# Optimization experiments

Measured on AMD Instinct MI355X. Metric: run time of the kernel, lower is better.

## Reference

```python
import jax, jax.numpy as jnp
import numpy as np

G, KS = 8, 3          # groups, kernel size
K = KS * KS           # sampling points per group
OM = 32               # per-group offset_mask dim: ceil(3K/8)*8
EPS = 1e-5


def setup_inputs() -> dict:
    key = jax.random.key(0)
    ks = jax.random.split(key, 12)
    N, C, H, W = 4, 128, 64, 64
    x = jax.random.normal(ks[0], (N, C, H, W), jnp.float32)
    w_value = jax.random.normal(ks[1], (C, C), jnp.float32) / np.sqrt(C)
    b_value = jax.random.normal(ks[2], (C,), jnp.float32) * 0.01
    # small offset weights -> modest sampling offsets (real module inits these to 0)
    w_off = jax.random.normal(ks[3], (C, G * OM), jnp.float32) * 0.02
    b_off = jax.random.normal(ks[4], (G * OM,), jnp.float32) * 0.01
    w_out = jax.random.normal(ks[5], (C, C), jnp.float32) / np.sqrt(C)
    b_out = jax.random.normal(ks[6], (C,), jnp.float32) * 0.01
    bn_gamma = jax.random.uniform(ks[7], (C,), jnp.float32, 0.5, 1.5)
    bn_beta = jax.random.normal(ks[8], (C,), jnp.float32) * 0.1
    bn_mean = jax.random.normal(ks[9], (C,), jnp.float32) * 0.1
    bn_var = jax.random.uniform(ks[10], (C,), jnp.float32, 0.5, 1.5)
    return dict(x=x, w_value=w_value, b_value=b_value, w_off=w_off, b_off=b_off,
                w_out=w_out, b_out=b_out, bn_gamma=bn_gamma, bn_beta=bn_beta,
                bn_mean=bn_mean, bn_var=bn_var)


def _dcnv4(x, w_value, b_value, w_off, b_off, w_out, b_out,
           bn_gamma, bn_beta, bn_mean, bn_var):
    N, C, H, W = x.shape
    Cg = C // G
    P = H * W
    xf = x.transpose(0, 2, 3, 1).reshape(N, P, C)              # N,P,C (channels-last tokens)
    val = xf @ w_value + b_value                               # value projection
    om = (xf @ w_off + b_off).reshape(N, P, G, OM)             # offsets+mask (padded to 32)
    offset = om[..., :2 * K].reshape(N, P, G, K, 2)            # (dx, dy) pairs
    mask = om[..., 2 * K:3 * K]                                # modulation, NO softmax (DCNv4)

    # base sampling grid: output pixel + centered 3x3 footprint (stride 1, dil 1)
    py, px = jnp.meshgrid(jnp.arange(H), jnp.arange(W), indexing='ij')
    kk = jnp.arange(KS) - (KS - 1) // 2
    ky, kx = jnp.meshgrid(kk, kk, indexing='ij')
    base_y = (py.reshape(-1)[:, None] + ky.reshape(-1)[None, :]).astype(x.dtype)  # P,K
    base_x = (px.reshape(-1)[:, None] + kx.reshape(-1)[None, :]).astype(x.dtype)
    sy = base_y[None, :, None, :] + offset[..., 1]             # N,P,G,K sampling y
    sx = base_x[None, :, None, :] + offset[..., 0]             # N,P,G,K sampling x

    vflat = val.reshape(N, P, G, Cg).transpose(0, 2, 1, 3)     # N,G,P,Cg

    def gather(iy, ix):
        lin = jnp.clip(iy, 0, H - 1) * W + jnp.clip(ix, 0, W - 1)   # N,P,G,K
        lin = lin.transpose(0, 2, 1, 3).reshape(N, G, P * K)
        g = jnp.take_along_axis(vflat, lin[..., None], axis=2)      # N,G,P*K,Cg
        return g.reshape(N, G, P, K, Cg).transpose(0, 2, 1, 3, 4)   # N,P,G,K,Cg

    y0 = jnp.floor(sy); x0 = jnp.floor(sx)
    ty = sy - y0; tx = sx - x0
    y0i = y0.astype(jnp.int32); x0i = x0.astype(jnp.int32)

    def valid(iy, ix):
        return ((iy >= 0) & (iy < H) & (ix >= 0) & (ix < W)).astype(x.dtype)

    acc = jnp.zeros((N, P, G, K, Cg), x.dtype)
    for dy, dx, wgt in ((0, 0, (1 - ty) * (1 - tx)), (0, 1, (1 - ty) * tx),
                        (1, 0, ty * (1 - tx)), (1, 1, ty * tx)):
        iy, ix = y0i + dy, x0i + dx
        acc = acc + gather(iy, ix) * (wgt * valid(iy, ix))[..., None]

    out = (acc * mask[..., None]).sum(axis=3)                  # aggregate over K -> N,P,G,Cg
    out = out.reshape(N, P, C) @ w_out + b_out                 # output projection
    out = out.reshape(N, H, W, C).transpose(0, 3, 1, 2)        # back to NCHW

    # BatchNorm (inference) + SiLU
    inv = bn_gamma / jnp.sqrt(bn_var + EPS)
    out = out * inv[None, :, None, None] + (bn_beta - bn_mean * inv)[None, :, None, None]
    return out * jax.nn.sigmoid(out)


def reference(x, w_value, b_value, w_off, b_off, w_out, b_out,
              bn_gamma, bn_beta, bn_mean, bn_var):
    return _dcnv4(x, w_value, b_value, w_off, b_off, w_out, b_out,
                  bn_gamma, bn_beta, bn_mean, bn_var)
```

## Files before the change

kernel.cpp:

```cpp
#include <hip/hip_runtime.h>
#include <cstdint>

typedef __bf16 v8bf __attribute__((ext_vector_type(8)));
typedef float f32x4 __attribute__((ext_vector_type(4)));

#define BN_EPS 1e-5f

__device__ __forceinline__ float b2f(uint32_t u) {
    union { uint32_t i; float f; } v; v.i = u << 16; return v.f;
}
__device__ __forceinline__ uint16_t f2b(float f) {
    uint32_t u = __builtin_bit_cast(uint32_t, f);
    u += 0x7fffu + ((u >> 16) & 1u);
    return (uint16_t)(u >> 16);
}

__global__ void prep_transpose_kernel(const float* __restrict__ x,
                                      const float* __restrict__ wv, const float* __restrict__ wo,
                                      const float* __restrict__ wout,
                                      uint16_t* __restrict__ xf, uint16_t* __restrict__ wT) {
    int bid = blockIdx.x;
    if (bid < 512) {
        __shared__ float lds[64 * 65];
        int cb = bid & 1, pb = (bid >> 1) & 63, n = bid >> 7;
        int c0 = cb * 64, p0 = pb * 64;
        int l = threadIdx.x & 63, q = threadIdx.x >> 6;
        const float* xp = x + ((size_t)(n * 128 + c0)) * 4096 + p0;
#pragma unroll
        for (int i = 0; i < 16; i++) {
            int c = i * 4 + q;
            lds[l * 65 + c] = xp[(size_t)c * 4096 + l];
        }
        __syncthreads();
#pragma unroll
        for (int i = 0; i < 16; i++) {
            int pr = i * 4 + q;
            xf[((size_t)(n * 4096 + p0 + pr)) * 128 + c0 + l] = f2b(lds[pr * 65 + l]);
        }
    } else {
        int idx = (bid - 512) * 256 + threadIdx.x;
        if (idx < 512 * 128) {
            int r = idx >> 7, ci = idx & 127;
            float v;
            if (r < 128)      v = wv[ci * 128 + r];
            else if (r < 384) v = wo[ci * 256 + (r - 128)];
            else              v = wout[ci * 128 + (r - 384)];
            wT[idx] = f2b(v);
        }
    }
}

__launch_bounds__(256)
__global__ void gemm1_kernel(const uint16_t* __restrict__ xf, const uint16_t* __restrict__ wT,
                             const float* __restrict__ b_value, const float* __restrict__ b_off,
                             uint16_t* __restrict__ valb, uint16_t* __restrict__ omb) {
    __shared__ __align__(16) uint16_t ldsX[128 * 136];
    __shared__ __align__(16) uint16_t ldsW[64 * 136];
    int ct = blockIdx.x;
    int pt = blockIdx.y;
    int p0 = pt * 128, cbase = ct * 64;
    int tid = threadIdx.x;
    int col16 = tid & 15, rowq = tid >> 4;

    const uint4* xg = (const uint4*)xf;
    uint4* lx = (uint4*)ldsX;
#pragma unroll
    for (int i = 0; i < 8; i++) {
        int row = i * 16 + rowq;
        lx[row * 17 + col16] = xg[(size_t)(p0 + row) * 16 + col16];
    }
    const uint4* wg = (const uint4*)wT;
    uint4* lw = (uint4*)ldsW;
#pragma unroll
    for (int i = 0; i < 4; i++) {
        int row = i * 16 + rowq;
        lw[row * 17 + col16] = wg[(size_t)(cbase + row) * 16 + col16];
    }
    __syncthreads();

    int wv = tid >> 6, lane = tid & 63;
    int ln = lane & 15, quad = lane >> 4;
    int cW = cbase + wv * 16 + quad * 4;
    f32x4 binit;
    if (cW < 128) binit = f32x4{b_value[cW], b_value[cW + 1], b_value[cW + 2], b_value[cW + 3]};
    else          binit = f32x4{b_off[cW - 128], b_off[cW - 127], b_off[cW - 126], b_off[cW - 125]};
    f32x4 acc[8];
#pragma unroll
    for (int t = 0; t < 8; t++) acc[t] = binit;

#pragma unroll
    for (int kk = 0; kk < 4; kk++) {
        v8bf a = *(const v8bf*)&ldsW[(wv * 16 + ln) * 136 + kk * 32 + quad * 8];
#pragma unroll
        for (int t = 0; t < 8; t++) {
            v8bf b = *(const v8bf*)&ldsX[(t * 16 + ln) * 136 + kk * 32 + quad * 8];
            acc[t] = __builtin_amdgcn_mfma_f32_16x16x32_bf16(a, b, acc[t], 0, 0, 0);
        }
    }

    int nimg = p0 >> 12, pin0 = p0 & 4095;
    if (cW < 128) {
        int g = cW >> 4, cg = cW & 15;
#pragma unroll
        for (int t = 0; t < 8; t++) {
            int p = pin0 + t * 16 + ln;
            uint32_t u0 = (uint32_t)f2b(acc[t][0]) | ((uint32_t)f2b(acc[t][1]) << 16);
            uint32_t u1 = (uint32_t)f2b(acc[t][2]) | ((uint32_t)f2b(acc[t][3]) << 16);
            *(uint2*)&valb[(((size_t)(nimg * 8 + g) * 4096 + p) << 4) + cg] = make_uint2(u0, u1);
        }
    } else {
        int j0 = cW - 128;
#pragma unroll
        for (int t = 0; t < 8; t++) {
            int p = pin0 + t * 16 + ln;
            uint32_t u0 = (uint32_t)f2b(acc[t][0]) | ((uint32_t)f2b(acc[t][1]) << 16);
            uint32_t u1 = (uint32_t)f2b(acc[t][2]) | ((uint32_t)f2b(acc[t][3]) << 16);
            *(uint2*)&omb[((size_t)(nimg * 4096 + p) << 8) + j0] = make_uint2(u0, u1);
        }
    }
}

__launch_bounds__(256)
__global__ void gather_gemm3_kernel(const uint16_t* __restrict__ omb, const uint16_t* __restrict__ valb,
                                    const uint16_t* __restrict__ wT,
                                    const float* __restrict__ b_out,
                                    const float* __restrict__ gamma, const float* __restrict__ beta,
                                    const float* __restrict__ mean, const float* __restrict__ var,
                                    float* __restrict__ out) {
    __shared__ __align__(16) uint16_t ldsA[16 * 136];
    __shared__ __align__(16) uint16_t ldsW[128 * 136];
    int pt = blockIdx.x;
    int p0 = pt * 16;
    int n = p0 >> 12, pin0 = p0 & 4095;
    int tid = threadIdx.x;

    {
        int col16 = tid & 15, rowq = tid >> 4;
        const uint4* wg = (const uint4*)wT;
        uint4* lw = (uint4*)ldsW;
#pragma unroll
        for (int i = 0; i < 8; i++) {
            int row = i * 16 + rowq;
            lw[row * 17 + col16] = wg[(size_t)(384 + row) * 16 + col16];
        }
    }

    int pl = tid & 15, g = (tid >> 4) & 7, h = tid >> 7;
    int p = p0 + pl;
    int pin = p & 4095;
    int py = pin >> 6, px = pin & 63;

    const uint16_t* op = omb + ((size_t)p << 8) + g * 32;
    uint4 q0 = *(const uint4*)(op);
    uint4 q1 = *(const uint4*)(op + 8);
    uint4 q2 = *(const uint4*)(op + 16);
    uint2 q3 = *(const uint2*)(op + 24);
    uint32_t w[14] = {q0.x, q0.y, q0.z, q0.w, q1.x, q1.y, q1.z, q1.w,
                      q2.x, q2.y, q2.z, q2.w, q3.x, q3.y};
    float o[28];
#pragma unroll
    for (int i = 0; i < 14; i++) { o[2 * i] = b2f(w[i] & 0xffff); o[2 * i + 1] = b2f(w[i] >> 16); }

    float acc[8];
#pragma unroll
    for (int i = 0; i < 8; i++) acc[i] = 0.f;

    const uint4* vb = (const uint4*)(valb + ((size_t)(n * 8 + g) << 16)) + h;
#pragma unroll
    for (int k = 0; k < 9; k++) {
        float sx = (float)(px + (k % 3) - 1) + o[2 * k];
        float sy = (float)(py + (k / 3) - 1) + o[2 * k + 1];
        float m = o[18 + k];
        float x0f = floorf(sx), y0f = floorf(sy);
        float tx = sx - x0f, ty = sy - y0f;
        int x0 = (int)x0f, y0 = (int)y0f;
        float wy[2] = {m * (1.f - ty), m * ty};
        float wx[2] = {1.f - tx, tx};
#pragma unroll
        for (int dy = 0; dy < 2; dy++) {
            int iy = y0 + dy;
            if (iy < 0 || iy > 63) continue;
#pragma unroll
            for (int dx = 0; dx < 2; dx++) {
                int ix = x0 + dx;
                if (ix < 0 || ix > 63) continue;
                float wgt = wy[dy] * wx[dx];
                uint4 v0 = vb[((size_t)(iy * 64 + ix)) * 2];
                acc[0] += wgt * b2f(v0.x & 0xffff); acc[1] += wgt * b2f(v0.x >> 16);
                acc[2] += wgt * b2f(v0.y & 0xffff); acc[3] += wgt * b2f(v0.y >> 16);
                acc[4] += wgt * b2f(v0.z & 0xffff); acc[5] += wgt * b2f(v0.z >> 16);
                acc[6] += wgt * b2f(v0.w & 0xffff); acc[7] += wgt * b2f(v0.w >> 16);
            }
        }
    }
    uint32_t u[4];
#pragma unroll
    for (int i = 0; i < 4; i++)
        u[i] = (uint32_t)f2b(acc[2 * i]) | ((uint32_t)f2b(acc[2 * i + 1]) << 16);
    *(uint4*)&ldsA[pl * 136 + g * 16 + h * 8] = make_uint4(u[0], u[1], u[2], u[3]);
    __syncthreads();

    int wv = tid >> 6, lane = tid & 63;
    int ln = lane & 15, quad = lane >> 4;
    f32x4 acc2[2];
#pragma unroll
    for (int t = 0; t < 2; t++) {
        float b = b_out[(wv * 2 + t) * 16 + ln];
        acc2[t] = f32x4{b, b, b, b};
    }
#pragma unroll
    for (int kk = 0; kk < 4; kk++) {
        v8bf a = *(const v8bf*)&ldsA[ln * 136 + kk * 32 + quad * 8];
#pragma unroll
        for (int t = 0; t < 2; t++) {
            v8bf b = *(const v8bf*)&ldsW[((wv * 2 + t) * 16 + ln) * 136 + kk * 32 + quad * 8];
            acc2[t] = __builtin_amdgcn_mfma_f32_16x16x32_bf16(a, b, acc2[t], 0, 0, 0);
        }
    }
    int pp = pin0 + quad * 4;
#pragma unroll
    for (int t = 0; t < 2; t++) {
        int cc = (wv * 2 + t) * 16 + ln;
        float inv = gamma[cc] * __frsqrt_rn(var[cc] + BN_EPS);
        float add = beta[cc] - mean[cc] * inv;
        float4 r;
        float* rp = &r.x;
#pragma unroll
        for (int q = 0; q < 4; q++) {
            float z = acc2[t][q] * inv + add;
            rp[q] = z / (1.f + __expf(-z));
        }
        *(float4*)&out[((size_t)(n * 128 + cc) << 12) + pp] = r;
    }
}

extern "C" void kernel_launch(void* const* d_in, const int* in_sizes, int n_in,
                              void* d_out, int out_size, void* d_ws, size_t ws_size,
                              hipStream_t stream) {
    const float* x       = (const float*)d_in[0];
    const float* w_value = (const float*)d_in[1];
    const float* b_value = (const float*)d_in[2];
    const float* w_off   = (const float*)d_in[3];
    const float* b_off   = (const float*)d_in[4];
    const float* w_out   = (const float*)d_in[5];
    const float* b_out   = (const float*)d_in[6];
    const float* gamma   = (const float*)d_in[7];
    const float* beta    = (const float*)d_in[8];
    const float* mean    = (const float*)d_in[9];
    const float* var     = (const float*)d_in[10];
    float* out = (float*)d_out;

    char* ws = (char*)d_ws;
    uint16_t* xf   = (uint16_t*)(ws);
    uint16_t* valb = (uint16_t*)(ws + ((size_t)8 << 20));
    uint16_t* omb  = (uint16_t*)(ws + ((size_t)12 << 20));
    uint16_t* wT   = (uint16_t*)(ws + ((size_t)20 << 20));

    hipLaunchKernelGGL(prep_transpose_kernel, dim3(768), dim3(256), 0, stream,
                       x, w_value, w_off, w_out, xf, wT);
    hipLaunchKernelGGL(gemm1_kernel, dim3(6, 128), dim3(256), 0, stream,
                       xf, wT, b_value, b_off, valb, omb);
    hipLaunchKernelGGL(gather_gemm3_kernel, dim3(1024), dim3(256), 0, stream,
                       omb, valb, wT, b_out, gamma, beta, mean, var, out);
}
```

Baseline: 112.4 us.

## Fuse NCHW transpose and bf16 cast into first GEMM, loop over output tiles

Drops the separate transpose pass that wrote a bf16 channels-last copy of x. Each gemm1 block now loads a 32-pixel strip of x straight from NCHW, converts it to bf16 in LDS, and loops over all six 64-column weight tiles. This removes the intermediate xf write and re-read, and stops x from being re-read once per column tile. In exchange, the 4-byte-per-lane global reads of x and the scalar LDS stores are less efficient, each block does only two MFMA tiles per weight load, and weights are reloaded for every pixel block.

```diff
diff --git a/kernel.cpp b/kernel.cpp
--- a/kernel.cpp
+++ b/kernel.cpp
@@ -15,107 +15,90 @@
     return (uint16_t)(u >> 16);
 }
 
-__global__ void prep_transpose_kernel(const float* __restrict__ x,
-                                      const float* __restrict__ wv, const float* __restrict__ wo,
-                                      const float* __restrict__ wout,
-                                      uint16_t* __restrict__ xf, uint16_t* __restrict__ wT) {
-    int bid = blockIdx.x;
-    if (bid < 512) {
-        __shared__ float lds[64 * 65];
-        int cb = bid & 1, pb = (bid >> 1) & 63, n = bid >> 7;
-        int c0 = cb * 64, p0 = pb * 64;
-        int l = threadIdx.x & 63, q = threadIdx.x >> 6;
-        const float* xp = x + ((size_t)(n * 128 + c0)) * 4096 + p0;
-#pragma unroll
-        for (int i = 0; i < 16; i++) {
-            int c = i * 4 + q;
-            lds[l * 65 + c] = xp[(size_t)c * 4096 + l];
-        }
-        __syncthreads();
-#pragma unroll
-        for (int i = 0; i < 16; i++) {
-            int pr = i * 4 + q;
-            xf[((size_t)(n * 4096 + p0 + pr)) * 128 + c0 + l] = f2b(lds[pr * 65 + l]);
-        }
-    } else {
-        int idx = (bid - 512) * 256 + threadIdx.x;
-        if (idx < 512 * 128) {
-            int r = idx >> 7, ci = idx & 127;
-            float v;
-            if (r < 128)      v = wv[ci * 128 + r];
-            else if (r < 384) v = wo[ci * 256 + (r - 128)];
-            else              v = wout[ci * 128 + (r - 384)];
-            wT[idx] = f2b(v);
-        }
-    }
+__global__ void prep_kernel(const float* __restrict__ wv, const float* __restrict__ wo,
+                            const float* __restrict__ wout, uint16_t* __restrict__ wT) {
+    int idx = blockIdx.x * 256 + threadIdx.x;
+    int r = idx >> 7, ci = idx & 127;
+    float v;
+    if (r < 128)      v = wv[ci * 128 + r];
+    else if (r < 384) v = wo[ci * 256 + (r - 128)];
+    else              v = wout[ci * 128 + (r - 384)];
+    wT[idx] = f2b(v);
 }
 
 __launch_bounds__(256)
-__global__ void gemm1_kernel(const uint16_t* __restrict__ xf, const uint16_t* __restrict__ wT,
+__global__ void gemm1_kernel(const float* __restrict__ x, const uint16_t* __restrict__ wT,
                              const float* __restrict__ b_value, const float* __restrict__ b_off,
                              uint16_t* __restrict__ valb, uint16_t* __restrict__ omb) {
-    __shared__ __align__(16) uint16_t ldsX[128 * 136];
+    __shared__ __align__(16) uint16_t ldsX[32 * 136];
     __shared__ __align__(16) uint16_t ldsW[64 * 136];
-    int ct = blockIdx.x;
-    int pt = blockIdx.y;
-    int p0 = pt * 128, cbase = ct * 64;
+    int pt = blockIdx.x;
+    int p0 = pt * 32;
+    int n = p0 >> 12, pin0 = p0 & 4095;
+    int py = pin0 >> 6, px0 = pin0 & 63;
     int tid = threadIdx.x;
+
+    {
+        int l = tid & 31, q = tid >> 5;
+        const float* xp = x + ((size_t)(n * 128)) * 4096 + py * 64 + px0;
+#pragma unroll
+        for (int i = 0; i < 16; i++) {
+            int c = i * 8 + q;
+            ldsX[l * 136 + c] = f2b(xp[(size_t)c * 4096 + l]);
+        }
+    }
+    __syncthreads();
+
+    int wv = tid >> 6, lane = tid & 63;
+    int ln = lane & 15, quad = lane >> 4;
     int col16 = tid & 15, rowq = tid >> 4;
-
-    const uint4* xg = (const uint4*)xf;
-    uint4* lx = (uint4*)ldsX;
-#pragma unroll
-    for (int i = 0; i < 8; i++) {
-        int row = i * 16 + rowq;
-        lx[row * 17 + col16] = xg[(size_t)(p0 + row) * 16 + col16];
-    }
     const uint4* wg = (const uint4*)wT;
     uint4* lw = (uint4*)ldsW;
-#pragma unroll
-    for (int i = 0; i < 4; i++) {
-        int row = i * 16 + rowq;
-        lw[row * 17 + col16] = wg[(size_t)(cbase + row) * 16 + col16];
-    }
-    __syncthreads();
-
-    int wv = tid >> 6, lane = tid & 63;
-    int ln = lane & 15, quad = lane >> 4;
-    int cW = cbase + wv * 16 + quad * 4;
-    f32x4 binit;
-    if (cW < 128) binit = f32x4{b_value[cW], b_value[cW + 1], b_value[cW + 2], b_value[cW + 3]};
-    else          binit = f32x4{b_off[cW - 128], b_off[cW - 127], b_off[cW - 126], b_off[cW - 125]};
-    f32x4 acc[8];
-#pragma unroll
-    for (int t = 0; t < 8; t++) acc[t] = binit;
-
-#pragma unroll
-    for (int kk = 0; kk < 4; kk++) {
-        v8bf a = *(const v8bf*)&ldsW[(wv * 16 + ln) * 136 + kk * 32 + quad * 8];
-#pragma unroll
-        for (int t = 0; t < 8; t++) {
-            v8bf b = *(const v8bf*)&ldsX[(t * 16 + ln) * 136 + kk * 32 + quad * 8];
-            acc[t] = __builtin_amdgcn_mfma_f32_16x16x32_bf16(a, b, acc[t], 0, 0, 0);
-        }
-    }
-
-    int nimg = p0 >> 12, pin0 = p0 & 4095;
-    if (cW < 128) {
-        int g = cW >> 4, cg = cW & 15;
-#pragma unroll
-        for (int t = 0; t < 8; t++) {
-            int p = pin0 + t * 16 + ln;
-            uint32_t u0 = (uint32_t)f2b(acc[t][0]) | ((uint32_t)f2b(acc[t][1]) << 16);
-            uint32_t u1 = (uint32_t)f2b(acc[t][2]) | ((uint32_t)f2b(acc[t][3]) << 16);
-            *(uint2*)&valb[(((size_t)(nimg * 8 + g) * 4096 + p) << 4) + cg] = make_uint2(u0, u1);
-        }
-    } else {
-        int j0 = cW - 128;
-#pragma unroll
-        for (int t = 0; t < 8; t++) {
-            int p = pin0 + t * 16 + ln;
-            uint32_t u0 = (uint32_t)f2b(acc[t][0]) | ((uint32_t)f2b(acc[t][1]) << 16);
-            uint32_t u1 = (uint32_t)f2b(acc[t][2]) | ((uint32_t)f2b(acc[t][3]) << 16);
-            *(uint2*)&omb[((size_t)(nimg * 4096 + p) << 8) + j0] = make_uint2(u0, u1);
+
+    for (int ct = 0; ct < 6; ct++) {
+        int cbase = ct * 64;
+        if (ct > 0) __syncthreads();
+#pragma unroll
+        for (int i = 0; i < 4; i++) {
+            int row = i * 16 + rowq;
+            lw[row * 17 + col16] = wg[(size_t)(cbase + row) * 16 + col16];
+        }
+        __syncthreads();
+
+        int cW = cbase + wv * 16 + quad * 4;
+        f32x4 binit;
+        if (cW < 128) binit = f32x4{b_value[cW], b_value[cW + 1], b_value[cW + 2], b_value[cW + 3]};
+        else          binit = f32x4{b_off[cW - 128], b_off[cW - 127], b_off[cW - 126], b_off[cW - 125]};
+        f32x4 acc[2] = {binit, binit};
+
+#pragma unroll
+        for (int kk = 0; kk < 4; kk++) {
+            v8bf a = *(const v8bf*)&ldsW[(wv * 16 + ln) * 136 + kk * 32 + quad * 8];
+#pragma unroll
+            for (int t = 0; t < 2; t++) {
+                v8bf b = *(const v8bf*)&ldsX[(t * 16 + ln) * 136 + kk * 32 + quad * 8];
+                acc[t] = __builtin_amdgcn_mfma_f32_16x16x32_bf16(a, b, acc[t], 0, 0, 0);
+            }
+        }
+
+        if (cW < 128) {
+            int g = cW >> 4, cg = cW & 15;
+#pragma unroll
+            for (int t = 0; t < 2; t++) {
+                int p = pin0 + t * 16 + ln;
+                uint32_t u0 = (uint32_t)f2b(acc[t][0]) | ((uint32_t)f2b(acc[t][1]) << 16);
+                uint32_t u1 = (uint32_t)f2b(acc[t][2]) | ((uint32_t)f2b(acc[t][3]) << 16);
+                *(uint2*)&valb[(((size_t)(n * 8 + g) * 4096 + p) << 4) + cg] = make_uint2(u0, u1);
+            }
+        } else {
+            int j0 = cW - 128;
+#pragma unroll
+            for (int t = 0; t < 2; t++) {
+                int p = pin0 + t * 16 + ln;
+                uint32_t u0 = (uint32_t)f2b(acc[t][0]) | ((uint32_t)f2b(acc[t][1]) << 16);
+                uint32_t u1 = (uint32_t)f2b(acc[t][2]) | ((uint32_t)f2b(acc[t][3]) << 16);
+                *(uint2*)&omb[((size_t)(n * 4096 + p) << 8) + j0] = make_uint2(u0, u1);
+            }
         }
     }
 }
@@ -251,15 +234,14 @@
     float* out = (float*)d_out;
 
     char* ws = (char*)d_ws;
-    uint16_t* xf   = (uint16_t*)(ws);
     uint16_t* valb = (uint16_t*)(ws + ((size_t)8 << 20));
     uint16_t* omb  = (uint16_t*)(ws + ((size_t)12 << 20));
     uint16_t* wT   = (uint16_t*)(ws + ((size_t)20 << 20));
 
-    hipLaunchKernelGGL(prep_transpose_kernel, dim3(768), dim3(256), 0, stream,
-                       x, w_value, w_off, w_out, xf, wT);
-    hipLaunchKernelGGL(gemm1_kernel, dim3(6, 128), dim3(256), 0, stream,
-                       xf, wT, b_value, b_off, valb, omb);
+    hipLaunchKernelGGL(prep_kernel, dim3(256), dim3(256), 0, stream,
+                       w_value, w_off, w_out, wT);
+    hipLaunchKernelGGL(gemm1_kernel, dim3(512), dim3(256), 0, stream,
+                       x, wT, b_value, b_off, valb, omb);
     hipLaunchKernelGGL(gather_gemm3_kernel, dim3(1024), dim3(256), 0, stream,
                        omb, valb, wT, b_out, gamma, beta, mean, var, out);
 }
```

New measurement: 111.9 us. No clear change (-0.4%).
